# Optimization experiments

Measured on AMD Instinct MI355X. Metric: run time of the kernel, lower is better.

Reference implementation:

```python
import jax, jax.numpy as jnp
import numpy as np

QMIN, QMAX = 0.0, 255.0
# activation statistics (min, max) per layer, from init_kwargs['stats']
STATS = {"conv1": (-0.5, 3.0), "conv2": (0.0, 6.0), "fc1": (0.0, 8.0), "fc2": (0.0, 10.0)}


def calc_scale_zp(min_val, max_val):
    scale = (max_val - min_val) / (QMAX - QMIN)
    # original: int(clamped initial zero point) -> truncation
    zp = jnp.trunc(jnp.clip(QMIN - min_val / scale, QMIN, QMAX))
    return scale, zp


def quantize(x, min_val=None, max_val=None):
    if min_val is None:
        min_val, max_val = x.min(), x.max()
    scale, zp = calc_scale_zp(min_val, max_val)
    q = jnp.round(jnp.clip(zp + x / scale, QMIN, QMAX))
    return q, scale, zp


def conv2d(x, w, b):
    y = jax.lax.conv_general_dilated(x, w, (1, 1), "VALID",
                                     dimension_numbers=("NCHW", "OIHW", "NCHW"))
    return y + b[None, :, None, None]


def linear(x, w, b):
    return x @ w.T + b


def max_pool_2x2(x):
    return jax.lax.reduce_window(x, -jnp.inf, jax.lax.max, (1, 1, 2, 2), (1, 1, 2, 2), "VALID")


def quantize_layer(q_x, scale_x, zp_x, W, B, apply_fn, stat):
    # fake-quant weights/bias with their own min/max
    wq, scale_w, zp_w = quantize(W)
    bq, scale_b, zp_b = quantize(B)
    scale_next, zp_next = calc_scale_zp(stat[0], stat[1])
    X = q_x - zp_x
    W_eff = scale_x * scale_w * (wq - zp_w)
    B_eff = scale_b * (bq + zp_b)  # '+ zp_b' is faithful to the source
    y = jax.nn.relu(apply_fn(X, W_eff, B_eff) / scale_next + zp_next)
    # .round().byte() in torch wraps mod 256
    return jnp.mod(jnp.round(y), 256.0), scale_next, zp_next


def setup_inputs() -> dict:
    key = jax.random.key(0)
    ks = jax.random.split(key, 9)
    B = 4096
    return {
        "x": jax.random.normal(ks[0], (B, 1, 28, 28), jnp.float32),
        "conv1_w": jax.random.normal(ks[1], (20, 1, 5, 5), jnp.float32) * 0.1,
        "conv1_b": jax.random.normal(ks[2], (20,), jnp.float32) * 0.1,
        "conv2_w": jax.random.normal(ks[3], (50, 20, 5, 5), jnp.float32) * 0.05,
        "conv2_b": jax.random.normal(ks[4], (50,), jnp.float32) * 0.05,
        "fc1_w": jax.random.normal(ks[5], (500, 800), jnp.float32) * 0.03,
        "fc1_b": jax.random.normal(ks[6], (500,), jnp.float32) * 0.03,
        "fc2_w": jax.random.normal(ks[7], (10, 500), jnp.float32) * 0.05,
        "fc2_b": jax.random.normal(ks[8], (10,), jnp.float32) * 0.05,
    }


def reference(x, conv1_w, conv1_b, conv2_w, conv2_b, fc1_w, fc1_b, fc2_w, fc2_b):
    q, s, zp = quantize(x, STATS["conv1"][0], STATS["conv1"][1])
    q, s, zp = quantize_layer(q, s, zp, conv1_w, conv1_b, conv2d, STATS["conv2"])
    q = max_pool_2x2(q)                       # [B,20,12,12]
    q, s, zp = quantize_layer(q, s, zp, conv2_w, conv2_b, conv2d, STATS["fc1"])
    q = max_pool_2x2(q)                       # [B,50,4,4]
    q = q.reshape(-1, 4 * 4 * 50)             # [B,800]
    q, s, zp = quantize_layer(q, s, zp, fc1_w, fc1_b, linear, STATS["fc2"])
    xf = s * (q - zp)                         # dequantize
    logits = linear(xf, fc2_w, fc2_b)         # [B,10]
    return jax.nn.log_softmax(logits, axis=1)
```

## Files before the change

kernel.cpp:

```cpp
#include <hip/hip_runtime.h>
#include <cmath>

#define TPB 256
typedef float floatx4 __attribute__((ext_vector_type(4)));
typedef __bf16 bf16x8 __attribute__((ext_vector_type(8)));
typedef unsigned short ushort8 __attribute__((ext_vector_type(8)));
typedef unsigned short ushort_t;

#define OFF_PMN 16
#define OFF_PMX 96
#define OFF_B1 520
#define OFF_B2 544
#define OFF_B3 600
#define W1BF_BYTE 6144
#define W2BF_BYTE 8192
#define W3BF_BYTE 131072
#define Q2_BYTE  29360128ULL
#define Q3_BYTE  1048576ULL

#define S_X1 (3.5f/255.0f)
#define ZP_X1 36.0f
#define S_N1 (6.0f/255.0f)
#define S_N2 (8.0f/255.0f)
#define S_N3 (10.0f/255.0f)

#define XSTR 40

__device__ inline float qclip(float x, float s, float zp){
    return rintf(fminf(fmaxf(zp + x / s, 0.0f), 255.0f));
}
__device__ inline ushort_t bfbits(float v){
    return (ushort_t)(__float_as_uint(v) >> 16);
}

__global__ __launch_bounds__(TPB) void k_minmax(
        const float* c1w, const float* c1b, const float* c2w, const float* c2b,
        const float* f1w, const float* f1b, float* pmn, float* pmx){
    __shared__ float smn[TPB], smx[TPB];
    int bb = blockIdx.x, tid = threadIdx.x;
    const float* src; int n, sub, nsub;
    if      (bb == 0){ src=c1w; n=500;    sub=0;     nsub=1;  }
    else if (bb == 1){ src=c1b; n=20;     sub=0;     nsub=1;  }
    else if (bb <  6){ src=c2w; n=25000;  sub=bb-2;  nsub=4;  }
    else if (bb == 6){ src=c2b; n=50;     sub=0;     nsub=1;  }
    else if (bb < 71){ src=f1w; n=400000; sub=bb-7;  nsub=64; }
    else             { src=f1b; n=500;    sub=0;     nsub=1;  }
    float mn = INFINITY, mx = -INFINITY;
    for (int i = sub*TPB + tid; i < n; i += nsub*TPB){
        float v = src[i]; mn = fminf(mn, v); mx = fmaxf(mx, v);
    }
    smn[tid] = mn; smx[tid] = mx; __syncthreads();
    for (int s = TPB/2; s > 0; s >>= 1){
        if (tid < s){
            smn[tid] = fminf(smn[tid], smn[tid+s]);
            smx[tid] = fmaxf(smx[tid], smx[tid+s]);
        }
        __syncthreads();
    }
    if (tid == 0){ pmn[bb] = smn[0]; pmx[bb] = smx[0]; }
}

#define N_EFF 452157
__global__ __launch_bounds__(TPB) void k_make_eff(
        const float* c1w, const float* c1b, const float* c2w, const float* c2b,
        const float* f1w, const float* f1b, const float* pmn, const float* pmx,
        float* ws, ushort_t* w1bf, ushort_t* w2bf, ushort_t* w3bf){
    __shared__ float sS[6], sZ[6];
    int tid = threadIdx.x;
    int wv = tid >> 6, lane = tid & 63;
    const int starts[6] = {0,1,2,6,7,71};
    const int counts[6] = {1,1,4,1,64,1};
    #pragma unroll
    for (int rep = 0; rep < 2; ++rep){
        int t = wv + rep*4;
        if (t < 6){
            float mn = INFINITY, mx = -INFINITY;
            if (lane < counts[t]){ mn = pmn[starts[t]+lane]; mx = pmx[starts[t]+lane]; }
            #pragma unroll
            for (int off = 32; off > 0; off >>= 1){
                mn = fminf(mn, __shfl_xor(mn, off));
                mx = fmaxf(mx, __shfl_xor(mx, off));
            }
            if (lane == 0){
                float s = (mx - mn) / 255.0f;
                sS[t] = s;
                sZ[t] = truncf(fminf(fmaxf(0.0f - mn / s, 0.0f), 255.0f));
            }
        }
    }
    __syncthreads();

    int i = blockIdx.x * TPB + tid;
    if (i >= N_EFF) return;
    if (i < 1024){
        int n = i >> 5, k = i & 31;
        float v = 0.0f;
        if (n < 20 && k < 25) v = qclip(c1w[n*25 + k], sS[0], sZ[0]) - sZ[0];
        w1bf[i] = bfbits(v);
    } else if (i < 1044){
        int j = i - 1024;
        ws[OFF_B1 + j] = (sS[1] * (qclip(c1b[j], sS[1], sZ[1]) + sZ[1])) / S_N1;
    } else if (i < 42004){
        int j = i - 1044;
        int c = j >> 11, r = j & 2047, co = r >> 5, k = r & 31;
        int q = k >> 3, jj = k & 7;
        int tap, ci; bool valid;
        if (c < 13){ tap = 2*c + (q>>1); ci = (q&1)*8 + jj; valid = (tap < 25); }
        else       { tap = 4*(c-13) + q; ci = 16 + jj;      valid = (tap < 25) && (jj < 4); }
        valid = valid && (co < 50);
        float v = 0.0f;
        if (valid) v = qclip(c2w[(co*20 + ci)*25 + tap], sS[2], sZ[2]) - sZ[2];
        w2bf[j] = bfbits(v);
    } else if (i < 42054){
        int j = i - 42004;
        ws[OFF_B2 + j] = (sS[3] * (qclip(c2b[j], sS[3], sZ[3]) + sZ[3])) / S_N2;
    } else if (i < 451654){
        int j = i - 42054;
        int n = j / 800, k = j - 800*n;
        float v = 0.0f;
        if (n < 500) v = qclip(f1w[n*800 + k], sS[4], sZ[4]) - sZ[4];
        w3bf[j] = bfbits(v);
    } else if (i < 452154){
        int j = i - 451654;
        ws[OFF_B3 + j] = (sS[5] * (qclip(f1b[j], sS[5], sZ[5]) + sZ[5])) / S_N3;
    } else if (i == 452154){
        ws[0] = (S_N1 * sS[2]) / S_N2;
    } else if (i == 452155){
        ws[1] = (S_N2 * sS[4]) / S_N3;
    } else {
        ws[2] = (S_X1 * sS[0]) / S_N1;
    }
}

__global__ __launch_bounds__(TPB) void k_conv12(const float* x, const ushort_t* w1bf,
                                                const ushort_t* w2bt, const float* ws,
                                                ushort_t* q2bf, int B){
    __shared__ __align__(16) ushort_t xs[144*XSTR];
    __shared__ ushort_t hbu[5760];
    ushort_t* xim = xs;
    int b = blockIdx.x, tid = threadIdx.x;
    int lane = tid & 63, wv = tid >> 6;
    int ln = lane & 15, quad = lane >> 4;

    const float* xb = x + (size_t)b * 784;
    for (int i = tid; i < 784; i += TPB){
        float v = xb[i];
        float q = rintf(fminf(fmaxf(ZP_X1 + v / S_X1, 0.0f), 255.0f));
        ushort_t bits = bfbits(q - ZP_X1);
        xim[i] = bits; xim[784 + i] = bits; xim[1568 + i] = bits; xim[2352 + i] = bits;
    }

    int offj[8]; bool vj[8];
    #pragma unroll
    for (int j = 0; j < 8; ++j){
        int k = quad*8 + j;
        vj[j] = (k < 25);
        int kh = k / 5, kw = k - 5*kh;
        offj[j] = vj[j] ? (kh*28 + kw) : 0;
    }
    const ushort_t* xq = xim + quad*784;

    ushort8 bw0 = *(const ushort8*)(w1bf + ln*32 + quad*8);
    ushort8 bw1 = *(const ushort8*)(w1bf + (16 + ln)*32 + quad*8);
    bf16x8 bf0 = __builtin_bit_cast(bf16x8, bw0);
    bf16x8 bf1 = __builtin_bit_cast(bf16x8, bw1);

    float K1 = ws[2];
    float B1_0 = ws[OFF_B1 + ln];
    float B1_1 = (ln < 4) ? ws[OFF_B1 + 16 + ln] : 0.0f;
    __syncthreads();

    for (int i = 0; i < 9; ++i){
        int mt = 9*wv + i;
        int m = mt*16 + ln;
        int oh = m / 24, ow = m - 24*oh;
        int base = oh*28 + ow;
        ushort8 aw;
        #pragma unroll
        for (int j = 0; j < 8; ++j)
            aw[j] = vj[j] ? xq[base + offj[j]] : (ushort_t)0;
        bf16x8 af = __builtin_bit_cast(bf16x8, aw);
        floatx4 z = (floatx4){0.f,0.f,0.f,0.f};
        floatx4 a0 = __builtin_amdgcn_mfma_f32_16x16x32_bf16(af, bf0, z, 0, 0, 0);
        floatx4 a1 = __builtin_amdgcn_mfma_f32_16x16x32_bf16(af, bf1, z, 0, 0, 0);

        int m0 = mt*16 + quad*4;
        int oh0 = m0 / 24, owp = (m0 - 24*oh0) >> 1;
        int hbase = (oh0*12 + owp)*20;
        {
            unsigned int qv[4];
            #pragma unroll
            for (int r = 0; r < 4; ++r){
                float y = fmaxf(fmaf(a0[r], K1, B1_0), 0.0f);
                qv[r] = ((unsigned int)rintf(y)) & 255u;
            }
            unsigned int h0 = qv[0] > qv[1] ? qv[0] : qv[1];
            unsigned int h1 = qv[2] > qv[3] ? qv[2] : qv[3];
            hbu[hbase + ln]      = (ushort_t)h0;
            hbu[hbase + 20 + ln] = (ushort_t)h1;
        }
        if (ln < 4){
            unsigned int qv[4];
            #pragma unroll
            for (int r = 0; r < 4; ++r){
                float y = fmaxf(fmaf(a1[r], K1, B1_1), 0.0f);
                qv[r] = ((unsigned int)rintf(y)) & 255u;
            }
            unsigned int h0 = qv[0] > qv[1] ? qv[0] : qv[1];
            unsigned int h1 = qv[2] > qv[3] ? qv[2] : qv[3];
            hbu[hbase + 16 + ln]      = (ushort_t)h0;
            hbu[hbase + 36 + ln]      = (ushort_t)h1;
        }
    }
    __syncthreads();

    for (int o = tid; o < 3456; o += TPB){
        int p = o / 24, c = o - 24*p;
        unsigned int m_ = 0;
        if (c < 20){
            int ph = p / 12, pw = p - 12*ph;
            unsigned int t_ = hbu[((2*ph)*12 + pw)*20 + c];
            unsigned int u_ = hbu[((2*ph+1)*12 + pw)*20 + c];
            m_ = t_ > u_ ? t_ : u_;
        }
        xs[p*XSTR + c] = bfbits((float)m_);
    }
    __syncthreads();

    int mt0 = (wv & 1) * 2;
    int nt0 = (wv >> 1) * 2;
    int abase[2];
    #pragma unroll
    for (int mi = 0; mi < 2; ++mi)
        abase[mi] = (24*(mt0+mi) + (ln>>3)*12 + (ln&7)) * XSTR;
    int aoff[20];
    #pragma unroll
    for (int c = 0; c < 20; ++c){
        int tap, inner;
        if (c < 13){ tap = 2*c + (quad>>1); inner = (quad&1)*8; }
        else       { tap = 4*(c-13) + quad; inner = 16; }
        int pt = 0;
        if (tap < 25){ int kh = tap/5, kw = tap-5*kh; pt = kh*12 + kw; }
        aoff[c] = pt*XSTR + inner;
    }

    float sc2d = ws[0];
    const ushort_t* bsrc0 = w2bt + (size_t)(nt0*16 + ln)*32 + quad*8;
    const ushort_t* bsrc1 = bsrc0 + 16*32;

    floatx4 acc[2][2];
    #pragma unroll
    for (int mi = 0; mi < 2; ++mi)
        #pragma unroll
        for (int ni = 0; ni < 2; ++ni) acc[mi][ni] = (floatx4){0.f,0.f,0.f,0.f};

    #pragma unroll
    for (int c = 0; c < 20; ++c){
        ushort8 b0w = *(const ushort8*)(bsrc0 + c*2048);
        ushort8 b1w = *(const ushort8*)(bsrc1 + c*2048);
        ushort8 a0w = *(const ushort8*)(xs + abase[0] + aoff[c]);
        ushort8 a1w = *(const ushort8*)(xs + abase[1] + aoff[c]);
        bf16x8 a0 = __builtin_bit_cast(bf16x8, a0w);
        bf16x8 a1 = __builtin_bit_cast(bf16x8, a1w);
        bf16x8 b0 = __builtin_bit_cast(bf16x8, b0w);
        bf16x8 b1 = __builtin_bit_cast(bf16x8, b1w);
        acc[0][0] = __builtin_amdgcn_mfma_f32_16x16x32_bf16(a0, b0, acc[0][0], 0, 0, 0);
        acc[0][1] = __builtin_amdgcn_mfma_f32_16x16x32_bf16(a0, b1, acc[0][1], 0, 0, 0);
        acc[1][0] = __builtin_amdgcn_mfma_f32_16x16x32_bf16(a1, b0, acc[1][0], 0, 0, 0);
        acc[1][1] = __builtin_amdgcn_mfma_f32_16x16x32_bf16(a1, b1, acc[1][1], 0, 0, 0);
    }

    #pragma unroll
    for (int ni = 0; ni < 2; ++ni){
        int co = (nt0 + ni)*16 + ln;
        float bias2d = (co < 50) ? ws[OFF_B2 + co] : 0.0f;
        #pragma unroll
        for (int mi = 0; mi < 2; ++mi){
            int mt = mt0 + mi;
            unsigned int qv[4];
            #pragma unroll
            for (int r = 0; r < 4; ++r){
                float y = fmaxf(fmaf(acc[mi][ni][r], sc2d, bias2d), 0.0f);
                qv[r] = ((unsigned int)rintf(y)) & 255u;
            }
            unsigned int h0 = qv[0] > qv[1] ? qv[0] : qv[1];
            unsigned int h1 = qv[2] > qv[3] ? qv[2] : qv[3];
            unsigned int p0 = (unsigned int)__shfl_xor((int)h0, 32);
            unsigned int p1 = (unsigned int)__shfl_xor((int)h1, 32);
            unsigned int v0 = h0 > p0 ? h0 : p0;
            unsigned int v1 = h1 > p1 ? h1 : p1;
            if (quad < 2 && co < 50){
                size_t base = (size_t)b*800 + co*16 + mt*4 + quad*2;
                q2bf[base]     = bfbits((float)v0);
                q2bf[base + 1] = bfbits((float)v1);
            }
        }
    }
}

__global__ __launch_bounds__(TPB) void k_fc1(const ushort_t* q2bf, const ushort_t* w3bf,
                                             const float* ws, unsigned char* q3, int B){
    __shared__ ushort_t As[2][64*40];
    int tid = threadIdx.x;
    int n0b = blockIdx.x * 64;
    int b0  = blockIdx.y * 64;
    int lane = tid & 63, wv = tid >> 6;
    int ln = lane & 15, quad = lane >> 4;
    int n0 = n0b + wv*16;
    int lrow = tid >> 2, lk = (tid & 3) * 8;
    const ushort_t* asrc = q2bf + (size_t)(b0 + lrow)*800 + lk;
    ushort_t* adst0 = &As[0][0] + lrow*40 + lk;
    ushort_t* adst1 = &As[1][0] + lrow*40 + lk;

    floatx4 acc[4];
    #pragma unroll
    for (int mt = 0; mt < 4; ++mt) acc[mt] = (floatx4){0.f,0.f,0.f,0.f};

    *(ushort8*)adst0 = *(const ushort8*)asrc;
    __syncthreads();

    for (int c = 0; c < 25; ++c){
        const ushort_t* cur = &As[c & 1][0];
        ushort8 tn;
        bool pf = (c + 1 < 25);
        if (pf) tn = *(const ushort8*)(asrc + (c + 1)*32);
        ushort8 bw = *(const ushort8*)(w3bf + (size_t)(n0 + ln)*800 + c*32 + quad*8);
        bf16x8 bfr = __builtin_bit_cast(bf16x8, bw);
        #pragma unroll
        for (int mt = 0; mt < 4; ++mt){
            ushort8 aw = *(const ushort8*)(cur + (16*mt + ln)*40 + quad*8);
            acc[mt] = __builtin_amdgcn_mfma_f32_16x16x32_bf16(
                          __builtin_bit_cast(bf16x8, aw), bfr, acc[mt], 0, 0, 0);
        }
        if (pf) *(ushort8*)(((c + 1) & 1) ? adst1 : adst0) = tn;
        __syncthreads();
    }

    float sc3d = ws[1];
    int n = n0 + ln;
    if (n < 500){
        float bias = ws[OFF_B3 + n];
        #pragma unroll
        for (int mt = 0; mt < 4; ++mt){
            #pragma unroll
            for (int r = 0; r < 4; ++r){
                int m = 16*mt + 4*quad + r;
                float y = fmaxf(fmaf(acc[mt][r], sc3d, bias), 0.0f);
                q3[(size_t)(b0 + m)*500 + n] = (unsigned char)(((unsigned int)rintf(y)) & 255u);
            }
        }
    }
}

__global__ __launch_bounds__(TPB) void k_fc2(const unsigned char* q3, const float* w2,
                                             const float* b2, float* out, int B){
    __shared__ float w2s[5000];
    __shared__ float b2s[10];
    int tid = threadIdx.x;
    for (int i = tid; i < 5000; i += TPB) w2s[i] = w2[i];
    if (tid < 10) b2s[tid] = b2[tid];
    __syncthreads();
    int lane = tid & 63, wv = tid >> 6;
    for (int rr = 0; rr < 4; ++rr){
        int b = blockIdx.x*16 + wv*4 + rr;
        if (b >= B) break;
        float acc[10];
        #pragma unroll
        for (int c = 0; c < 10; ++c) acc[c] = 0.0f;
        for (int k = lane; k < 500; k += 64){
            float xf = S_N3 * (float)q3[(size_t)b*500 + k];
            #pragma unroll
            for (int c = 0; c < 10; ++c)
                acc[c] = fmaf(xf, w2s[c*500 + k], acc[c]);
        }
        #pragma unroll
        for (int off = 32; off > 0; off >>= 1)
            #pragma unroll
            for (int c = 0; c < 10; ++c)
                acc[c] += __shfl_xor(acc[c], off);
        float lg[10], m = -INFINITY;
        #pragma unroll
        for (int c = 0; c < 10; ++c){ lg[c] = acc[c] + b2s[c]; m = fmaxf(m, lg[c]); }
        float sum = 0.0f;
        #pragma unroll
        for (int c = 0; c < 10; ++c) sum += expf(lg[c] - m);
        float ls = logf(sum);
        if (lane < 10) out[(size_t)b*10 + lane] = lg[lane] - m - ls;
    }
}

extern "C" void kernel_launch(void* const* d_in, const int* in_sizes, int n_in,
                              void* d_out, int out_size, void* d_ws, size_t ws_size,
                              hipStream_t stream){
    const float* x   = (const float*)d_in[0];
    const float* c1w = (const float*)d_in[1];
    const float* c1b = (const float*)d_in[2];
    const float* c2w = (const float*)d_in[3];
    const float* c2b = (const float*)d_in[4];
    const float* f1w = (const float*)d_in[5];
    const float* f1b = (const float*)d_in[6];
    const float* f2w = (const float*)d_in[7];
    const float* f2b = (const float*)d_in[8];
    int B = in_sizes[0] / 784;

    float* ws = (float*)d_ws;
    float* pmn = ws + OFF_PMN;
    float* pmx = ws + OFF_PMX;
    ushort_t* w1bf = (ushort_t*)((char*)d_ws + W1BF_BYTE);
    ushort_t* w2bf = (ushort_t*)((char*)d_ws + W2BF_BYTE);
    ushort_t* w3bf = (ushort_t*)((char*)d_ws + W3BF_BYTE);
    ushort_t* q2bf = (ushort_t*)((char*)d_ws + Q2_BYTE);
    unsigned char* q3 = (unsigned char*)d_ws + Q3_BYTE;
    float* out = (float*)d_out;

    k_minmax<<<72, TPB, 0, stream>>>(c1w, c1b, c2w, c2b, f1w, f1b, pmn, pmx);
    k_make_eff<<<(N_EFF + TPB - 1)/TPB, TPB, 0, stream>>>(c1w, c1b, c2w, c2b, f1w, f1b, pmn, pmx, ws, w1bf, w2bf, w3bf);
    k_conv12<<<B, TPB, 0, stream>>>(x, w1bf, w2bf, ws, q2bf, B);
    dim3 g_fc1(8, B/64);
    k_fc1<<<g_fc1, TPB, 0, stream>>>(q2bf, w3bf, ws, q3, B);
    k_fc2<<<(B + 15)/16, TPB, 0, stream>>>(q3, f2w, f2b, out, B);
}
```

Measured before the change: 174.1 us.

## Drop LDS staging in fc1 and load A tiles directly with smaller batch tile

The fc1 GEMM kernel no longer double-buffers the activation tile through shared memory with per-chunk barriers. Each wave now loads its A and B fragments straight from global memory, and the batch tile shrinks from 64 to 32 rows, so the grid has twice as many blocks. This removes the LDS traffic and the barriers and raises parallelism. In exchange, the four waves of a block now each re-read the same activation rows from global memory or cache, and each wave has fewer MFMAs per load.

```diff
diff --git a/kernel.cpp b/kernel.cpp
--- a/kernel.cpp
+++ b/kernel.cpp
@@ -300,40 +300,30 @@
 
 __global__ __launch_bounds__(TPB) void k_fc1(const ushort_t* q2bf, const ushort_t* w3bf,
                                              const float* ws, unsigned char* q3, int B){
-    __shared__ ushort_t As[2][64*40];
     int tid = threadIdx.x;
-    int n0b = blockIdx.x * 64;
-    int b0  = blockIdx.y * 64;
     int lane = tid & 63, wv = tid >> 6;
     int ln = lane & 15, quad = lane >> 4;
-    int n0 = n0b + wv*16;
-    int lrow = tid >> 2, lk = (tid & 3) * 8;
-    const ushort_t* asrc = q2bf + (size_t)(b0 + lrow)*800 + lk;
-    ushort_t* adst0 = &As[0][0] + lrow*40 + lk;
-    ushort_t* adst1 = &As[1][0] + lrow*40 + lk;
-
-    floatx4 acc[4];
-    #pragma unroll
-    for (int mt = 0; mt < 4; ++mt) acc[mt] = (floatx4){0.f,0.f,0.f,0.f};
-
-    *(ushort8*)adst0 = *(const ushort8*)asrc;
-    __syncthreads();
-
+    int n0 = blockIdx.x * 64 + wv*16;
+    int b0 = blockIdx.y * 32;
+
+    const ushort_t* bsrc = w3bf + (size_t)(n0 + ln)*800 + quad*8;
+    const ushort_t* asrc0 = q2bf + (size_t)(b0 + ln)*800 + quad*8;
+    const ushort_t* asrc1 = q2bf + (size_t)(b0 + 16 + ln)*800 + quad*8;
+
+    floatx4 acc[2];
+    #pragma unroll
+    for (int mt = 0; mt < 2; ++mt) acc[mt] = (floatx4){0.f,0.f,0.f,0.f};
+
+    #pragma unroll
     for (int c = 0; c < 25; ++c){
-        const ushort_t* cur = &As[c & 1][0];
-        ushort8 tn;
-        bool pf = (c + 1 < 25);
-        if (pf) tn = *(const ushort8*)(asrc + (c + 1)*32);
-        ushort8 bw = *(const ushort8*)(w3bf + (size_t)(n0 + ln)*800 + c*32 + quad*8);
+        ushort8 bw  = *(const ushort8*)(bsrc  + c*32);
+        ushort8 a0w = *(const ushort8*)(asrc0 + c*32);
+        ushort8 a1w = *(const ushort8*)(asrc1 + c*32);
         bf16x8 bfr = __builtin_bit_cast(bf16x8, bw);
-        #pragma unroll
-        for (int mt = 0; mt < 4; ++mt){
-            ushort8 aw = *(const ushort8*)(cur + (16*mt + ln)*40 + quad*8);
-            acc[mt] = __builtin_amdgcn_mfma_f32_16x16x32_bf16(
-                          __builtin_bit_cast(bf16x8, aw), bfr, acc[mt], 0, 0, 0);
-        }
-        if (pf) *(ushort8*)(((c + 1) & 1) ? adst1 : adst0) = tn;
-        __syncthreads();
+        acc[0] = __builtin_amdgcn_mfma_f32_16x16x32_bf16(
+                     __builtin_bit_cast(bf16x8, a0w), bfr, acc[0], 0, 0, 0);
+        acc[1] = __builtin_amdgcn_mfma_f32_16x16x32_bf16(
+                     __builtin_bit_cast(bf16x8, a1w), bfr, acc[1], 0, 0, 0);
     }
 
     float sc3d = ws[1];
@@ -341,7 +331,7 @@
     if (n < 500){
         float bias = ws[OFF_B3 + n];
         #pragma unroll
-        for (int mt = 0; mt < 4; ++mt){
+        for (int mt = 0; mt < 2; ++mt){
             #pragma unroll
             for (int r = 0; r < 4; ++r){
                 int m = 16*mt + 4*quad + r;
@@ -416,7 +406,7 @@
     k_minmax<<<72, TPB, 0, stream>>>(c1w, c1b, c2w, c2b, f1w, f1b, pmn, pmx);
     k_make_eff<<<(N_EFF + TPB - 1)/TPB, TPB, 0, stream>>>(c1w, c1b, c2w, c2b, f1w, f1b, pmn, pmx, ws, w1bf, w2bf, w3bf);
     k_conv12<<<B, TPB, 0, stream>>>(x, w1bf, w2bf, ws, q2bf, B);
-    dim3 g_fc1(8, B/64);
+    dim3 g_fc1(8, (B + 31)/32);
     k_fc1<<<g_fc1, TPB, 0, stream>>>(q2bf, w3bf, ws, q3, B);
     k_fc2<<<(B + 15)/16, TPB, 0, stream>>>(q3, f2w, f2b, out, B);
 }
```

Measured after the change: 173.3 us. No clear change (-0.5%).
